# Kernel tuning notes

Hardware: AMD Instinct MI355X
Metric: run time of the kernel (lower is better)

## Reference

```python
import jax, jax.numpy as jnp
import numpy as np

D = 1024      # config.input_dim
H = 16        # config.num_heads
EPS = 1e-6    # layernorm epsilon


def setup_inputs() -> dict:
    key = jax.random.key(0)
    ks = jax.random.split(key, 12)
    B, S = 4, 2048
    s = 1.0 / np.sqrt(D)
    return {
        "Q": jax.random.normal(ks[0], (B, S, D), jnp.float32),
        "K": jax.random.normal(ks[1], (B, S, D), jnp.float32),
        "V": jax.random.normal(ks[2], (B, S, D), jnp.float32),
        "Wq": jax.random.normal(ks[3], (D, D), jnp.float32) * s,
        "bq": jnp.zeros((D,), jnp.float32),
        "Wk": jax.random.normal(ks[4], (D, D), jnp.float32) * s,
        "bk": jnp.zeros((D,), jnp.float32),
        "Wv": jax.random.normal(ks[5], (D, D), jnp.float32) * s,
        "bv": jnp.zeros((D,), jnp.float32),
        "Wo": jax.random.normal(ks[6], (D, D), jnp.float32) * s,
        "bo": jnp.zeros((D,), jnp.float32),
        "gamma": jnp.ones((D,), jnp.float32),
        "beta": jnp.zeros((D,), jnp.float32),
    }


def _layernorm(x, gamma, beta):
    mu = jnp.mean(x, axis=-1, keepdims=True)
    var = jnp.mean(jnp.square(x - mu), axis=-1, keepdims=True)
    return (x - mu) * jax.lax.rsqrt(var + EPS) * gamma + beta


def reference(Q, K, V, Wq, bq, Wk, bk, Wv, bv, Wo, bo, gamma, beta):
    # Type == 'D': pre-norm projections, causal MHA (no 1/sqrt(d) scaling,
    # faithful to source), out projection, residual. Dropout = identity (eval).
    B, S, _ = Q.shape
    dh = D // H
    clone_Q = Q
    q = _layernorm(Q, gamma, beta) @ Wq + bq
    k = _layernorm(K, gamma, beta) @ Wk + bk
    v = _layernorm(V, gamma, beta) @ Wv + bv
    # [B, S, D] -> [B, H, S, dh]
    q = q.reshape(B, S, H, dh).transpose(0, 2, 1, 3)
    k = k.reshape(B, S, H, dh).transpose(0, 2, 1, 3)
    v = v.reshape(B, S, H, dh).transpose(0, 2, 1, 3)
    score = jnp.einsum("bhsd,bhtd->bhst", q, k)  # [B, H, S, S]
    causal = jnp.tril(jnp.ones((S, S), bool))
    score = jnp.where(causal, score, -jnp.inf)
    attn = jax.nn.softmax(score, axis=-1)
    out = jnp.einsum("bhst,bhtd->bhsd", attn, v)  # [B, H, S, dh]
    out = out.transpose(0, 2, 1, 3).reshape(B, S, D)
    return clone_Q + (out @ Wo + bo)
```

## Files before the change

### kernel.cpp

```cpp
#include <hip/hip_runtime.h>
#include <hip/hip_bf16.h>

typedef __attribute__((ext_vector_type(8))) __bf16 bf16x8;
typedef __attribute__((ext_vector_type(4))) float f32x4;

union BF8U { uint4 u; bf16x8 b; };

static __device__ __forceinline__ unsigned short f2bf(float f){
  __bf16 h = (__bf16)f;
  return *reinterpret_cast<unsigned short*>(&h);
}

static __device__ __forceinline__ bf16x8 ld_bf8(const unsigned short* p){
  BF8U u; u.u = *reinterpret_cast<const uint4*>(p); return u.b;
}

static __device__ __forceinline__ f32x4 mfma16(bf16x8 a, bf16x8 b, f32x4 c){
  return __builtin_amdgcn_mfma_f32_16x16x32_bf16(a, b, c, 0, 0, 0);
}

static __device__ __forceinline__ void gl_lds16(const unsigned short* g, unsigned short* l){
  __builtin_amdgcn_global_load_lds(
      (const __attribute__((address_space(1))) unsigned int*)g,
      (__attribute__((address_space(3))) unsigned int*)l, 16, 0, 0);
}

__global__ __launch_bounds__(256) void prep_kernel(
    const float* __restrict__ Q, const float* __restrict__ K, const float* __restrict__ V,
    const float* __restrict__ gamma, const float* __restrict__ beta,
    unsigned short* __restrict__ lnQ, unsigned short* __restrict__ lnK,
    unsigned short* __restrict__ lnV,
    const float* __restrict__ Wq, const float* __restrict__ Wk,
    const float* __restrict__ Wv, const float* __restrict__ Wo,
    unsigned short* __restrict__ WtQ, unsigned short* __restrict__ WtK,
    unsigned short* __restrict__ WtV, unsigned short* __restrict__ WtO)
{
  __shared__ __align__(16) unsigned short smem[64*72];
  const int bid = (int)blockIdx.x;
  const int t = threadIdx.x;
  if (bid < 24576){
    const int sel = bid >> 13;
    const int row = bid & 8191;
    const float* X = sel==0 ? Q : sel==1 ? K : V;
    unsigned short* out = sel==0 ? lnQ : sel==1 ? lnK : lnV;
    float* red = reinterpret_cast<float*>(smem);
    const float4 x = reinterpret_cast<const float4*>(X + (size_t)row*1024)[t];
    float s  = x.x + x.y + x.z + x.w;
    float ss = x.x*x.x + x.y*x.y + x.z*x.z + x.w*x.w;
    for (int off = 1; off < 64; off <<= 1){
      s  += __shfl_xor(s, off);
      ss += __shfl_xor(ss, off);
    }
    const int wv = t >> 6;
    if ((t & 63) == 0){ red[wv] = s; red[4 + wv] = ss; }
    __syncthreads();
    s  = red[0] + red[1] + red[2] + red[3];
    ss = red[4] + red[5] + red[6] + red[7];
    const float mu   = s * (1.0f/1024.0f);
    const float var  = ss * (1.0f/1024.0f) - mu*mu;
    const float rstd = rsqrtf(var + 1e-6f);
    const float4 gm = reinterpret_cast<const float4*>(gamma)[t];
    const float4 bt = reinterpret_cast<const float4*>(beta)[t];
    unsigned short pk[4];
    pk[0] = f2bf((x.x - mu)*rstd*gm.x + bt.x);
    pk[1] = f2bf((x.y - mu)*rstd*gm.y + bt.y);
    pk[2] = f2bf((x.z - mu)*rstd*gm.z + bt.z);
    pk[3] = f2bf((x.w - mu)*rstd*gm.w + bt.w);
    *reinterpret_cast<uint2*>(out + (size_t)row*1024 + t*4) = *reinterpret_cast<uint2*>(pk);
  } else {
    const int wid = bid - 24576;
    const int wsel = wid >> 8;
    const float* W = wsel==0 ? Wq : wsel==1 ? Wk : wsel==2 ? Wv : Wo;
    unsigned short* Wt = wsel==0 ? WtQ : wsel==1 ? WtK : wsel==2 ? WtV : WtO;
    unsigned short (*tile)[72] = reinterpret_cast<unsigned short(*)[72]>(smem);
    const int tb = wid & 255;
    const int bk = (tb >> 4) * 64;
    const int bn = (tb & 15) * 64;
    {
      const int kr = t >> 2, nc0 = (t & 3) * 16;
      const float4* src = reinterpret_cast<const float4*>(W + (size_t)(bk + kr)*1024 + bn + nc0);
      for (int q = 0; q < 4; ++q){
        float4 vv = src[q];
        tile[kr][nc0 + q*4 + 0] = f2bf(vv.x);
        tile[kr][nc0 + q*4 + 1] = f2bf(vv.y);
        tile[kr][nc0 + q*4 + 2] = f2bf(vv.z);
        tile[kr][nc0 + q*4 + 3] = f2bf(vv.w);
      }
    }
    __syncthreads();
    {
      const int nr = t >> 2, kc0 = (t & 3) * 16;
      unsigned short outv[16];
      for (int j = 0; j < 16; ++j) outv[j] = tile[kc0 + j][nr];
      uint4* dst = reinterpret_cast<uint4*>(Wt + (size_t)(bn + nr)*1024 + bk + kc0);
      dst[0] = reinterpret_cast<uint4*>(outv)[0];
      dst[1] = reinterpret_cast<uint4*>(outv)[1];
    }
  }
}

__global__ __launch_bounds__(256) void qkv_kernel(
    const unsigned short* __restrict__ lnQ, const unsigned short* __restrict__ lnK,
    const unsigned short* __restrict__ lnV,
    const unsigned short* __restrict__ WtQ, const unsigned short* __restrict__ WtK,
    const unsigned short* __restrict__ WtV,
    const float* __restrict__ bq, const float* __restrict__ bk,
    const float* __restrict__ bv,
    unsigned short* __restrict__ qb, unsigned short* __restrict__ kb,
    unsigned short* __restrict__ vtb)
{
  __shared__ unsigned short a_lds[128][64];
  __shared__ unsigned short b_lds[128][64];
  const int bid = (int)blockIdx.x;
  const int which = bid >> 9;
  const int inner = bid & 511;
  const unsigned short* A  = which==0 ? lnQ : which==1 ? lnK : lnV;
  const unsigned short* Bt = which==0 ? WtQ : which==1 ? WtK : WtV;
  const float* bias = which==0 ? bq : which==1 ? bk : bv;

  const int t = threadIdx.x;
  const int lane = t & 63;
  const int w = t >> 6;
  const int g = lane >> 4, c = lane & 15;
  const int bm = inner >> 3, bn = inner & 7;
  const int wr = w >> 1, wc = w & 1;
  const int row0 = bm * 128, col0 = bn * 128;

  f32x4 acc[4][4];
  const f32x4 fz = {0.f, 0.f, 0.f, 0.f};
  for (int i = 0; i < 4; ++i) for (int j = 0; j < 4; ++j) acc[i][j] = fz;

  for (int kb_ = 0; kb_ < 1024; kb_ += 64){
    for (int i = 0; i < 4; ++i){
      const int cid = t + i*256;
      const int r = cid >> 3, ch = cid & 7;
      const int chs = (ch ^ (r & 7)) * 8;
      gl_lds16(&A [(size_t)(row0 + r)*1024 + kb_ + chs], &a_lds[0][0] + cid*8);
      gl_lds16(&Bt[(size_t)(col0 + r)*1024 + kb_ + chs], &b_lds[0][0] + cid*8);
    }
    __syncthreads();
    bf16x8 af[4][2], bfr[4][2];
    for (int mt = 0; mt < 4; ++mt)
      for (int kc = 0; kc < 2; ++kc){
        const int R = wr*64 + mt*16 + c;
        af[mt][kc] = ld_bf8(&a_lds[R][((kc*4 + g) ^ (R & 7))*8]);
      }
    for (int nt = 0; nt < 4; ++nt)
      for (int kc = 0; kc < 2; ++kc){
        const int R = wc*64 + nt*16 + c;
        bfr[nt][kc] = ld_bf8(&b_lds[R][((kc*4 + g) ^ (R & 7))*8]);
      }
    for (int kc = 0; kc < 2; ++kc)
      for (int mt = 0; mt < 4; ++mt)
        for (int nt = 0; nt < 4; ++nt)
          acc[mt][nt] = mfma16(af[mt][kc], bfr[nt][kc], acc[mt][nt]);
    __syncthreads();
  }

  const float scale = (which == 0) ? 1.4426950408889634f : 1.0f;
  unsigned short* outb = which==0 ? qb : kb;
  for (int mt = 0; mt < 4; ++mt){
    for (int nt = 0; nt < 4; ++nt){
      const int gcol = col0 + wc*64 + nt*16 + c;
      const float bv_ = bias[gcol];
      const int hh = gcol >> 6, d = gcol & 63;
      if (which == 2){
        const int grow0 = row0 + wr*64 + mt*16 + g*4;
        const int bidx = grow0 >> 11, s0 = grow0 & 2047;
        unsigned short pk[4];
        for (int r = 0; r < 4; ++r) pk[r] = f2bf(acc[mt][nt][r] + bv_);
        *reinterpret_cast<uint2*>(&vtb[((size_t)((bidx*16 + hh)*64 + d))*2048 + s0]) =
          *reinterpret_cast<uint2*>(pk);
      } else {
        for (int r = 0; r < 4; ++r){
          const int grow = row0 + wr*64 + mt*16 + g*4 + r;
          const int bidx = grow >> 11, s = grow & 2047;
          outb[((size_t)(bidx*16 + hh)*2048 + s)*64 + d] = f2bf((acc[mt][nt][r] + bv_)*scale);
        }
      }
    }
  }
}

__global__ __launch_bounds__(256) void ogemm_kernel(
    const unsigned short* __restrict__ A,
    const unsigned short* __restrict__ Bt,
    const float* __restrict__ bias,
    const float* __restrict__ residual,
    float* __restrict__ outf)
{
  __shared__ unsigned short a_lds[128][64];
  __shared__ unsigned short b_lds[128][64];
  const int t = threadIdx.x;
  const int lane = t & 63;
  const int w = t >> 6;
  const int g = lane >> 4, c = lane & 15;
  const int bm = (int)blockIdx.x >> 3, bn = (int)blockIdx.x & 7;
  const int wr = w >> 1, wc = w & 1;
  const int row0 = bm * 128, col0 = bn * 128;

  f32x4 acc[4][4];
  const f32x4 fz = {0.f, 0.f, 0.f, 0.f};
  for (int i = 0; i < 4; ++i) for (int j = 0; j < 4; ++j) acc[i][j] = fz;

  for (int kb_ = 0; kb_ < 1024; kb_ += 64){
    for (int i = 0; i < 4; ++i){
      const int cid = t + i*256;
      const int r = cid >> 3, ch = cid & 7;
      const int chs = (ch ^ (r & 7)) * 8;
      gl_lds16(&A [(size_t)(row0 + r)*1024 + kb_ + chs], &a_lds[0][0] + cid*8);
      gl_lds16(&Bt[(size_t)(col0 + r)*1024 + kb_ + chs], &b_lds[0][0] + cid*8);
    }
    __syncthreads();
    bf16x8 af[4][2], bfr[4][2];
    for (int mt = 0; mt < 4; ++mt)
      for (int kc = 0; kc < 2; ++kc){
        const int R = wr*64 + mt*16 + c;
        af[mt][kc] = ld_bf8(&a_lds[R][((kc*4 + g) ^ (R & 7))*8]);
      }
    for (int nt = 0; nt < 4; ++nt)
      for (int kc = 0; kc < 2; ++kc){
        const int R = wc*64 + nt*16 + c;
        bfr[nt][kc] = ld_bf8(&b_lds[R][((kc*4 + g) ^ (R & 7))*8]);
      }
    for (int kc = 0; kc < 2; ++kc)
      for (int mt = 0; mt < 4; ++mt)
        for (int nt = 0; nt < 4; ++nt)
          acc[mt][nt] = mfma16(af[mt][kc], bfr[nt][kc], acc[mt][nt]);
    __syncthreads();
  }

  for (int mt = 0; mt < 4; ++mt){
    for (int nt = 0; nt < 4; ++nt){
      const int gcol = col0 + wc*64 + nt*16 + c;
      const float bv_ = bias[gcol];
      for (int r = 0; r < 4; ++r){
        const int grow = row0 + wr*64 + mt*16 + g*4 + r;
        const size_t idx = (size_t)grow*1024 + gcol;
        outf[idx] = acc[mt][nt][r] + bv_ + residual[idx];
      }
    }
  }
}

__global__ __launch_bounds__(512, 4) void attn_kernel(
    const unsigned short* __restrict__ qg,
    const unsigned short* __restrict__ kg,
    const unsigned short* __restrict__ vtg,
    unsigned short* __restrict__ og)
{
  __shared__ unsigned short k_lds[64][64];
  __shared__ unsigned short vt_lds[64][64];
  __shared__ unsigned short p_lds[8][16][72];
  const int t = threadIdx.x;
  const int lane = t & 63;
  const int w = t >> 6;
  const int g = lane >> 4, c = lane & 15;
  const int bh = (int)blockIdx.x & 63;
  const int p  = (int)blockIdx.x >> 6;
  const size_t base = (size_t)bh * 2048 * 64;
  const int bidx = bh >> 4, hh = bh & 15;
  const float NEG = -__builtin_inff();
  const f32x4 fz = {0.f,0.f,0.f,0.f};

  const int sr = t >> 3, sch = t & 7;
  const int schs = (sch ^ (sr & 7)) * 8;

  for (int half = 0; half < 2; ++half){
    const int qb_ = half ? (15 - p) : p;
    const int qw = qb_*128 + w*16;

    bf16x8 qf[2];
    for (int kc = 0; kc < 2; ++kc)
      qf[kc] = ld_bf8(&qg[base + (size_t)(qw + c)*64 + kc*32 + g*8]);

    f32x4 o_acc[4];
    for (int i = 0; i < 4; ++i) o_acc[i] = fz;
    float m_run = NEG, l_run = 0.f;

    const int nkv = qb_*2 + 2;
    for (int kvt = 0; kvt < nkv; ++kvt){
      const int kv0 = kvt * 64;
      gl_lds16(&kg [base + (size_t)(kv0 + sr)*64 + schs], &k_lds[0][0]  + t*8);
      gl_lds16(&vtg[base + (size_t)sr*2048 + kv0 + schs], &vt_lds[0][0] + t*8);
      __syncthreads();

      if (kv0 <= qw + 15){
        bf16x8 kf[4][2];
        for (int ni = 0; ni < 4; ++ni)
          for (int kc = 0; kc < 2; ++kc){
            const int R = ni*16 + c;
            kf[ni][kc] = ld_bf8(&k_lds[R][((kc*4 + g) ^ (R & 7))*8]);
          }
        f32x4 st[4];
        for (int i = 0; i < 4; ++i) st[i] = fz;
        __builtin_amdgcn_s_setprio(1);
        for (int kc = 0; kc < 2; ++kc)
          for (int ni = 0; ni < 4; ++ni)
            st[ni] = mfma16(kf[ni][kc], qf[kc], st[ni]);
        __builtin_amdgcn_s_setprio(0);

        const int qglob = qw + c;
        float tmax = NEG;
        if (kv0 + 63 > qw){
          for (int ni = 0; ni < 4; ++ni)
            for (int r = 0; r < 4; ++r){
              const int kvglob = kv0 + ni*16 + g*4 + r;
              float sv = (kvglob <= qglob) ? st[ni][r] : NEG;
              st[ni][r] = sv;
              tmax = fmaxf(tmax, sv);
            }
        } else {
          for (int ni = 0; ni < 4; ++ni)
            for (int r = 0; r < 4; ++r)
              tmax = fmaxf(tmax, st[ni][r]);
        }
        tmax = fmaxf(tmax, __shfl_xor(tmax, 16));
        tmax = fmaxf(tmax, __shfl_xor(tmax, 32));

        const bool defer = __all(tmax - m_run <= 11.5f);
        if (!defer){
          const float m_new = fmaxf(m_run, tmax);
          const float alpha = __builtin_amdgcn_exp2f(m_run - m_new);
          m_run = m_new;
          l_run *= alpha;
          for (int ni = 0; ni < 4; ++ni){
            o_acc[ni][0] *= alpha; o_acc[ni][1] *= alpha;
            o_acc[ni][2] *= alpha; o_acc[ni][3] *= alpha;
          }
        }
        float tsum = 0.f;
        for (int ni = 0; ni < 4; ++ni){
          unsigned short pk[4];
          for (int r = 0; r < 4; ++r){
            const float pe = __builtin_amdgcn_exp2f(st[ni][r] - m_run);
            tsum += pe;
            pk[r] = f2bf(pe);
          }
          *reinterpret_cast<uint2*>(&p_lds[w][c][ni*16 + g*4]) =
            *reinterpret_cast<uint2*>(pk);
        }
        tsum += __shfl_xor(tsum, 16);
        tsum += __shfl_xor(tsum, 32);
        l_run += tsum;

        bf16x8 vf[4][2], pf[2];
        for (int ni = 0; ni < 4; ++ni)
          for (int kc = 0; kc < 2; ++kc){
            const int R = ni*16 + c;
            vf[ni][kc] = ld_bf8(&vt_lds[R][((kc*4 + g) ^ (R & 7))*8]);
          }
        for (int kc = 0; kc < 2; ++kc)
          pf[kc] = ld_bf8(&p_lds[w][c][kc*32 + g*8]);
        __builtin_amdgcn_s_setprio(1);
        for (int kc = 0; kc < 2; ++kc)
          for (int ni = 0; ni < 4; ++ni)
            o_acc[ni] = mfma16(vf[ni][kc], pf[kc], o_acc[ni]);
        __builtin_amdgcn_s_setprio(0);
      }
      __syncthreads();
    }

    const float invl = 1.0f / l_run;
    const int s = qw + c;
    const size_t obase = ((size_t)(bidx*2048 + s))*1024 + hh*64;
    for (int ni = 0; ni < 4; ++ni){
      unsigned short pk[4];
      pk[0] = f2bf(o_acc[ni][0]*invl);
      pk[1] = f2bf(o_acc[ni][1]*invl);
      pk[2] = f2bf(o_acc[ni][2]*invl);
      pk[3] = f2bf(o_acc[ni][3]*invl);
      *reinterpret_cast<uint2*>(&og[obase + ni*16 + g*4]) =
        *reinterpret_cast<uint2*>(pk);
    }
  }
}

extern "C" void kernel_launch(void* const* d_in, const int* in_sizes, int n_in,
                              void* d_out, int out_size, void* d_ws, size_t ws_size,
                              hipStream_t stream)
{
  (void)in_sizes; (void)n_in; (void)out_size;
  const float* Q  = (const float*)d_in[0];
  const float* K  = (const float*)d_in[1];
  const float* V  = (const float*)d_in[2];
  const float* Wq = (const float*)d_in[3];
  const float* bq = (const float*)d_in[4];
  const float* Wk = (const float*)d_in[5];
  const float* bk = (const float*)d_in[6];
  const float* Wv = (const float*)d_in[7];
  const float* bv = (const float*)d_in[8];
  const float* Wo = (const float*)d_in[9];
  const float* bo = (const float*)d_in[10];
  const float* gamma = (const float*)d_in[11];
  const float* beta  = (const float*)d_in[12];

  const size_t MB = 1024ull*1024ull;
  if (ws_size < 104*MB) return;
  char* ws = (char*)d_ws;
  unsigned short* lnQ = (unsigned short*)(ws + 0*MB);
  unsigned short* lnK = (unsigned short*)(ws + 16*MB);
  unsigned short* lnV = (unsigned short*)(ws + 32*MB);
  unsigned short* attn_out = lnQ;
  unsigned short* WtQ = (unsigned short*)(ws + 48*MB);
  unsigned short* WtK = (unsigned short*)(ws + 50*MB);
  unsigned short* WtV = (unsigned short*)(ws + 52*MB);
  unsigned short* WtO = (unsigned short*)(ws + 54*MB);
  unsigned short* qb  = (unsigned short*)(ws + 56*MB);
  unsigned short* kb  = (unsigned short*)(ws + 72*MB);
  unsigned short* vtb = (unsigned short*)(ws + 88*MB);
  float* out = (float*)d_out;

  prep_kernel<<<25600, 256, 0, stream>>>(Q, K, V, gamma, beta, lnQ, lnK, lnV,
                                         Wq, Wk, Wv, Wo, WtQ, WtK, WtV, WtO);
  qkv_kernel<<<1536, 256, 0, stream>>>(lnQ, lnK, lnV, WtQ, WtK, WtV,
                                       bq, bk, bv, qb, kb, vtb);
  attn_kernel<<<512, 512, 0, stream>>>(qb, kb, vtb, attn_out);
  ogemm_kernel<<<512, 256, 0, stream>>>(attn_out, WtO, bo, Q, out);
}
```

Measured before the change: 336.9 us.

## Shrink attention blocks to 64 query rows and swizzle block order across kernels

The attention kernel now uses 256-thread blocks covering 64 query rows each, launched as 1024 blocks with paired causal tiles. Each block loads 64-key tiles with two loads per thread, and the old per-warp skip of fully masked tiles is dropped because every tile up to the diagonal is now needed. The QKV and output GEMMs, and the attention grid, get a block-index swizzle so that consecutive blocks share weight or head data, aiming for better cache locality. The cost is that each K/V tile is reused by fewer query rows, so there are more K/V loads and more block-wide barriers per unit of work.

```diff
diff --git a/kernel.cpp b/kernel.cpp
--- a/kernel.cpp
+++ b/kernel.cpp
@@ -114,6 +114,7 @@
   const int bid = (int)blockIdx.x;
   const int which = bid >> 9;
   const int inner = bid & 511;
+  const int swz = ((inner & 7) << 6) | (inner >> 3);
   const unsigned short* A  = which==0 ? lnQ : which==1 ? lnK : lnV;
   const unsigned short* Bt = which==0 ? WtQ : which==1 ? WtK : WtV;
   const float* bias = which==0 ? bq : which==1 ? bk : bv;
@@ -122,7 +123,7 @@
   const int lane = t & 63;
   const int w = t >> 6;
   const int g = lane >> 4, c = lane & 15;
-  const int bm = inner >> 3, bn = inner & 7;
+  const int bm = swz >> 3, bn = swz & 7;
   const int wr = w >> 1, wc = w & 1;
   const int row0 = bm * 128, col0 = bn * 128;
 
@@ -192,10 +193,12 @@
   __shared__ unsigned short a_lds[128][64];
   __shared__ unsigned short b_lds[128][64];
   const int t = threadIdx.x;
+  const int inner = (int)blockIdx.x;
+  const int swz = ((inner & 7) << 6) | (inner >> 3);
   const int lane = t & 63;
   const int w = t >> 6;
   const int g = lane >> 4, c = lane & 15;
-  const int bm = (int)blockIdx.x >> 3, bn = (int)blockIdx.x & 7;
+  const int bm = swz >> 3, bn = swz & 7;
   const int wr = w >> 1, wc = w & 1;
   const int row0 = bm * 128, col0 = bn * 128;
 
@@ -243,7 +246,7 @@
   }
 }
 
-__global__ __launch_bounds__(512, 4) void attn_kernel(
+__global__ __launch_bounds__(256) void attn_kernel(
     const unsigned short* __restrict__ qg,
     const unsigned short* __restrict__ kg,
     const unsigned short* __restrict__ vtg,
@@ -251,24 +254,23 @@
 {
   __shared__ unsigned short k_lds[64][64];
   __shared__ unsigned short vt_lds[64][64];
-  __shared__ unsigned short p_lds[8][16][72];
+  __shared__ unsigned short p_lds[4][16][72];
   const int t = threadIdx.x;
   const int lane = t & 63;
   const int w = t >> 6;
   const int g = lane >> 4, c = lane & 15;
-  const int bh = (int)blockIdx.x & 63;
-  const int p  = (int)blockIdx.x >> 6;
+  const int orig = (int)blockIdx.x;
+  const int swz = ((orig & 7) << 7) | (orig >> 3);
+  const int bh = swz >> 4;
+  const int p  = swz & 15;
   const size_t base = (size_t)bh * 2048 * 64;
   const int bidx = bh >> 4, hh = bh & 15;
   const float NEG = -__builtin_inff();
   const f32x4 fz = {0.f,0.f,0.f,0.f};
 
-  const int sr = t >> 3, sch = t & 7;
-  const int schs = (sch ^ (sr & 7)) * 8;
-
   for (int half = 0; half < 2; ++half){
-    const int qb_ = half ? (15 - p) : p;
-    const int qw = qb_*128 + w*16;
+    const int qb_ = half ? (31 - p) : p;
+    const int qw = qb_*64 + w*16;
 
     bf16x8 qf[2];
     for (int kc = 0; kc < 2; ++kc)
@@ -278,86 +280,90 @@
     for (int i = 0; i < 4; ++i) o_acc[i] = fz;
     float m_run = NEG, l_run = 0.f;
 
-    const int nkv = qb_*2 + 2;
+    const int nkv = qb_ + 1;
     for (int kvt = 0; kvt < nkv; ++kvt){
       const int kv0 = kvt * 64;
-      gl_lds16(&kg [base + (size_t)(kv0 + sr)*64 + schs], &k_lds[0][0]  + t*8);
-      gl_lds16(&vtg[base + (size_t)sr*2048 + kv0 + schs], &vt_lds[0][0] + t*8);
+      for (int i = 0; i < 2; ++i){
+        const int cid = t + i*256;
+        const int r = cid >> 3, ch = cid & 7;
+        const int chs = (ch ^ (r & 7)) * 8;
+        gl_lds16(&kg [base + (size_t)(kv0 + r)*64 + chs], &k_lds[0][0]  + cid*8);
+        gl_lds16(&vtg[base + (size_t)r*2048 + kv0 + chs], &vt_lds[0][0] + cid*8);
+      }
       __syncthreads();
 
-      if (kv0 <= qw + 15){
-        bf16x8 kf[4][2];
+      bf16x8 kf[4][2];
+      for (int ni = 0; ni < 4; ++ni)
+        for (int kc = 0; kc < 2; ++kc){
+          const int R = ni*16 + c;
+          kf[ni][kc] = ld_bf8(&k_lds[R][((kc*4 + g) ^ (R & 7))*8]);
+        }
+      f32x4 st[4];
+      for (int i = 0; i < 4; ++i) st[i] = fz;
+      __builtin_amdgcn_s_setprio(1);
+      for (int kc = 0; kc < 2; ++kc)
         for (int ni = 0; ni < 4; ++ni)
-          for (int kc = 0; kc < 2; ++kc){
-            const int R = ni*16 + c;
-            kf[ni][kc] = ld_bf8(&k_lds[R][((kc*4 + g) ^ (R & 7))*8]);
+          st[ni] = mfma16(kf[ni][kc], qf[kc], st[ni]);
+      __builtin_amdgcn_s_setprio(0);
+
+      const int qglob = qw + c;
+      float tmax = NEG;
+      if (kvt == qb_){
+        for (int ni = 0; ni < 4; ++ni)
+          for (int r = 0; r < 4; ++r){
+            const int kvglob = kv0 + ni*16 + g*4 + r;
+            float sv = (kvglob <= qglob) ? st[ni][r] : NEG;
+            st[ni][r] = sv;
+            tmax = fmaxf(tmax, sv);
           }
-        f32x4 st[4];
-        for (int i = 0; i < 4; ++i) st[i] = fz;
-        __builtin_amdgcn_s_setprio(1);
-        for (int kc = 0; kc < 2; ++kc)
-          for (int ni = 0; ni < 4; ++ni)
-            st[ni] = mfma16(kf[ni][kc], qf[kc], st[ni]);
-        __builtin_amdgcn_s_setprio(0);
-
-        const int qglob = qw + c;
-        float tmax = NEG;
-        if (kv0 + 63 > qw){
-          for (int ni = 0; ni < 4; ++ni)
-            for (int r = 0; r < 4; ++r){
-              const int kvglob = kv0 + ni*16 + g*4 + r;
-              float sv = (kvglob <= qglob) ? st[ni][r] : NEG;
-              st[ni][r] = sv;
-              tmax = fmaxf(tmax, sv);
-            }
-        } else {
-          for (int ni = 0; ni < 4; ++ni)
-            for (int r = 0; r < 4; ++r)
-              tmax = fmaxf(tmax, st[ni][r]);
+      } else {
+        for (int ni = 0; ni < 4; ++ni)
+          for (int r = 0; r < 4; ++r)
+            tmax = fmaxf(tmax, st[ni][r]);
+      }
+      tmax = fmaxf(tmax, __shfl_xor(tmax, 16));
+      tmax = fmaxf(tmax, __shfl_xor(tmax, 32));
+
+      const bool defer = __all(tmax - m_run <= 11.5f);
+      if (!defer){
+        const float m_new = fmaxf(m_run, tmax);
+        const float alpha = __builtin_amdgcn_exp2f(m_run - m_new);
+        m_run = m_new;
+        l_run *= alpha;
+        for (int ni = 0; ni < 4; ++ni){
+          o_acc[ni][0] *= alpha; o_acc[ni][1] *= alpha;
+          o_acc[ni][2] *= alpha; o_acc[ni][3] *= alpha;
         }
-        tmax = fmaxf(tmax, __shfl_xor(tmax, 16));
-        tmax = fmaxf(tmax, __shfl_xor(tmax, 32));
-
-        const bool defer = __all(tmax - m_run <= 11.5f);
-        if (!defer){
-          const float m_new = fmaxf(m_run, tmax);
-          const float alpha = __builtin_amdgcn_exp2f(m_run - m_new);
-          m_run = m_new;
-          l_run *= alpha;
-          for (int ni = 0; ni < 4; ++ni){
-            o_acc[ni][0] *= alpha; o_acc[ni][1] *= alpha;
-            o_acc[ni][2] *= alpha; o_acc[ni][3] *= alpha;
-          }
+      }
+      float tsum = 0.f;
+      for (int ni = 0; ni < 4; ++ni){
+        unsigned short pk[4];
+        for (int r = 0; r < 4; ++r){
+          const float pe = __builtin_amdgcn_exp2f(st[ni][r] - m_run);
+          tsum += pe;
+          pk[r] = f2bf(pe);
         }
-        float tsum = 0.f;
-        for (int ni = 0; ni < 4; ++ni){
-          unsigned short pk[4];
-          for (int r = 0; r < 4; ++r){
-            const float pe = __builtin_amdgcn_exp2f(st[ni][r] - m_run);
-            tsum += pe;
-            pk[r] = f2bf(pe);
-          }
-          *reinterpret_cast<uint2*>(&p_lds[w][c][ni*16 + g*4]) =
-            *reinterpret_cast<uint2*>(pk);
+        *reinterpret_cast<uint2*>(&p_lds[w][c][ni*16 + g*4]) =
+          *reinterpret_cast<uint2*>(pk);
+      }
+      tsum += __shfl_xor(tsum, 16);
+      tsum += __shfl_xor(tsum, 32);
+      l_run += tsum;
+
+      bf16x8 vf[4][2], pf[2];
+      for (int ni = 0; ni < 4; ++ni)
+        for (int kc = 0; kc < 2; ++kc){
+          const int R = ni*16 + c;
+          vf[ni][kc] = ld_bf8(&vt_lds[R][((kc*4 + g) ^ (R & 7))*8]);
         }
-        tsum += __shfl_xor(tsum, 16);
-        tsum += __shfl_xor(tsum, 32);
-        l_run += tsum;
-
-        bf16x8 vf[4][2], pf[2];
+      for (int kc = 0; kc < 2; ++kc)
+        pf[kc] = ld_bf8(&p_lds[w][c][kc*32 + g*8]);
+      __builtin_amdgcn_s_setprio(1);
+      for (int kc = 0; kc < 2; ++kc)
         for (int ni = 0; ni < 4; ++ni)
-          for (int kc = 0; kc < 2; ++kc){
-            const int R = ni*16 + c;
-            vf[ni][kc] = ld_bf8(&vt_lds[R][((kc*4 + g) ^ (R & 7))*8]);
-          }
-        for (int kc = 0; kc < 2; ++kc)
-          pf[kc] = ld_bf8(&p_lds[w][c][kc*32 + g*8]);
-        __builtin_amdgcn_s_setprio(1);
-        for (int kc = 0; kc < 2; ++kc)
-          for (int ni = 0; ni < 4; ++ni)
-            o_acc[ni] = mfma16(vf[ni][kc], pf[kc], o_acc[ni]);
-        __builtin_amdgcn_s_setprio(0);
-      }
+          o_acc[ni] = mfma16(vf[ni][kc], pf[kc], o_acc[ni]);
+      __builtin_amdgcn_s_setprio(0);
+
       __syncthreads();
     }
 
@@ -415,6 +421,6 @@
                                          Wq, Wk, Wv, Wo, WtQ, WtK, WtV, WtO);
   qkv_kernel<<<1536, 256, 0, stream>>>(lnQ, lnK, lnV, WtQ, WtK, WtV,
                                        bq, bk, bv, qb, kb, vtb);
-  attn_kernel<<<512, 512, 0, stream>>>(qb, kb, vtb, attn_out);
+  attn_kernel<<<1024, 256, 0, stream>>>(qb, kb, vtb, attn_out);
   ogemm_kernel<<<512, 256, 0, stream>>>(attn_out, WtO, bo, Q, out);
 }
```

Measured after the change: 351.1 us. 4.2% more time.
